# Optimization experiments

Measured on AMD Instinct MI355X. Metric: run time of the kernel, lower is better.

The kernel has to match this reference:

```python
import jax, jax.numpy as jnp
import numpy as np
from jax import lax

NSTEPS = 7
BN_EPS = 1e-5


def setup_inputs() -> dict:
    key = jax.random.key(0)
    ks = jax.random.split(key, 7)
    bs, in_ch, h, w, k = 8, 16, 256, 256, 3
    f = jax.random.normal(ks[0], (bs, in_ch, h, w), dtype=jnp.float32)
    vec_w = jax.random.normal(ks[1], (2 * in_ch, in_ch, k, k), dtype=jnp.float32) * 0.1
    vec_b = jax.random.normal(ks[2], (2 * in_ch,), dtype=jnp.float32) * 0.1
    bn_gamma = jnp.ones((2 * in_ch,), dtype=jnp.float32)
    bn_beta = jnp.zeros((2 * in_ch,), dtype=jnp.float32)
    fuse_w = jax.random.normal(ks[3], (in_ch, in_ch, NSTEPS, 1, 1), dtype=jnp.float32) * 0.1
    fuse_b = jax.random.normal(ks[4], (in_ch,), dtype=jnp.float32) * 0.1
    return {"f": f, "vec_w": vec_w, "vec_b": vec_b, "bn_gamma": bn_gamma,
            "bn_beta": bn_beta, "fuse_w": fuse_w, "fuse_b": fuse_b}


def _bilinear_sample(src, py, px):
    """Bilinear sample with zero padding (torch grid_sample align_corners=True).
    src: [N,C,H,W]; py,px: [N,H,W] pixel coordinates (row, col)."""
    N, C, H, W = src.shape
    y0 = jnp.floor(py); x0 = jnp.floor(px)
    wy1 = py - y0; wy0 = 1.0 - wy1
    wx1 = px - x0; wx0 = 1.0 - wx1
    src_flat = src.reshape(N, C, H * W)

    def gather(yi, xi):
        valid = (yi >= 0) & (yi <= H - 1) & (xi >= 0) & (xi <= W - 1)
        yc = jnp.clip(yi, 0, H - 1).astype(jnp.int32)
        xc = jnp.clip(xi, 0, W - 1).astype(jnp.int32)
        idx = (yc * W + xc).reshape(N, 1, H * W)
        vals = jnp.take_along_axis(src_flat, idx, axis=2).reshape(N, C, H, W)
        return vals * valid.astype(src.dtype)[:, None, :, :]

    out = (wy0 * wx0)[:, None] * gather(y0, x0) \
        + (wy0 * wx1)[:, None] * gather(y0, x0 + 1) \
        + (wy1 * wx0)[:, None] * gather(y0 + 1, x0) \
        + (wy1 * wx1)[:, None] * gather(y0 + 1, x0 + 1)
    return out


def _warp(src, flow, grid_y, grid_x):
    # grid + flow in pixel space; original normalizes to [-1,1] then grid_sample
    # un-normalizes with align_corners=True, which is exactly pixel coords grid+flow.
    py = grid_y[None] + flow[:, 0]
    px = grid_x[None] + flow[:, 1]
    return _bilinear_sample(src, py, px)


def reference(f, vec_w, vec_b, bn_gamma, bn_beta, fuse_w, fuse_b):
    bs, in_ch, h, w = f.shape
    # vec_conv + BatchNorm2d (training-mode batch stats, biased variance)
    vec = lax.conv_general_dilated(f, vec_w, (1, 1), [(1, 1), (1, 1)],
                                   dimension_numbers=("NCHW", "OIHW", "NCHW"))
    vec = vec + vec_b[None, :, None, None]
    mean = vec.mean(axis=(0, 2, 3))
    var = vec.var(axis=(0, 2, 3))
    vec = bn_gamma[None, :, None, None] * (vec - mean[None, :, None, None]) \
        * lax.rsqrt(var + BN_EPS)[None, :, None, None] + bn_beta[None, :, None, None]

    c = vec.shape[1]  # = 2*in_ch
    vec = vec.reshape(bs * c // 2, 2, h, w)  # per-channel 2D flow fields

    grid_y, grid_x = jnp.meshgrid(jnp.arange(h, dtype=f.dtype),
                                  jnp.arange(w, dtype=f.dtype), indexing="ij")

    # VecInt: scaling and squaring, keeping every intermediate deformation
    vec = vec * (1.0 / 2 ** NSTEPS)
    deforms = []
    for _ in range(NSTEPS):
        vec = vec + _warp(vec, vec, grid_y, grid_x)
        deforms.append(vec)

    fsrc = f.reshape(bs * in_ch, 1, h, w)
    maps = [_warp(fsrc, d, grid_y, grid_x).reshape(bs, in_ch, h, w) for d in deforms]
    stacked = jnp.stack(maps, axis=2)  # [bs, in_ch, nsteps, h, w]

    # Conv3d with kernel (nsteps,1,1) then squeeze -> per-pixel channel/step mix
    out = jnp.einsum("ocs,bcshw->bohw", fuse_w[:, :, :, 0, 0], stacked)
    out = out + fuse_b[None, :, None, None]
    return out
```

## Files before the change

kernel.cpp:

```cpp
#include <hip/hip_runtime.h>
#include <hip/hip_fp16.h>

#define H 256
#define W 256
#define BS 8
#define IC 16
#define OCH 32
#define NSTEPS 7
#define PLANE (H*W)
#define NFIELDS (BS*IC)
#define BN_N (BS*PLANE)
#define BN_EPS 1e-5f
#define PW 260
#define PSZ (260 * 260)

__global__ void transpose_w_kernel(const float* __restrict__ w,
                                   __half2* __restrict__ wTh) {
    for (int idx = threadIdx.x; idx < IC * 9 * 16; idx += blockDim.x) {
        int rc = idx >> 4;
        int p  = idx & 15;
        float lo = w[(2 * p) * (IC * 9) + rc];
        float hi = w[(2 * p + 1) * (IC * 9) + rc];
        wTh[idx] = __floats2half2_rn(lo, hi);
    }
}

__global__ void guard_zero_kernel(unsigned* __restrict__ bufA,
                                  unsigned* __restrict__ bufB,
                                  unsigned short* __restrict__ f16p) {
    int p = blockIdx.x;
    size_t pb = (size_t)p * PSZ;
    for (int i = threadIdx.x; i < 2064; i += blockDim.x) {
        int row, col;
        if (i < 1040) {
            int r = i / 260;
            row = (r == 0) ? 0 : 256 + r;
            col = i - r * 260;
        } else {
            int j = i - 1040;
            int c = j / 256;
            col = (c == 0) ? 0 : 256 + c;
            row = 1 + (j - c * 256);
        }
        size_t off = pb + (size_t)row * PW + col;
        bufA[off] = 0u;
        bufB[off] = 0u;
        f16p[off] = 0;
    }
}

__global__ __launch_bounds__(256) void dup_kernel(const float* __restrict__ f,
                                                  __half* __restrict__ f16p) {
    int blk = blockIdx.x;
    int p  = blk >> 3;
    int r0 = (blk & 7) * 32;
    const float* fp = f + (size_t)p * PLANE;
    __half* dp = f16p + (size_t)p * PSZ;
    int tx = threadIdx.x;
#pragma unroll 4
    for (int ry = 0; ry < 32; ++ry) {
        int y = r0 + ry;
        dp[(size_t)(y + 1) * PW + tx + 1] = __float2half(fp[(size_t)y * W + tx]);
    }
}

__global__ __launch_bounds__(256, 8) void conv_kernel(
    const float* __restrict__ f, const __half2* __restrict__ wTh,
    const float* __restrict__ vec_b, __half2* __restrict__ vec_out) {
    __shared__ __align__(16) __half sf[16][10][40];

    int blk = blockIdx.x;
    int xcd = blk & 7;
    int i   = blk >> 3;
    int b   = i >> 5;
    int j   = i & 31;
    int ty0 = ((xcd << 2) | (j >> 3)) * 8;
    int tx0 = (j & 7) * 32;
    int tid = threadIdx.x;

    {
        int sic = tid >> 4;
        int st  = tid & 15;
        if (st < 10) {
            int gx0 = tx0 - 4 + 4 * st;
            const float* fpl = f + (size_t)(b * IC + sic) * PLANE;
            bool full = (gx0 >= 0) && (gx0 + 3 < W);
#pragma unroll
            for (int r = 0; r < 10; ++r) {
                int gy = ty0 - 1 + r;
                float4 v = make_float4(0.f, 0.f, 0.f, 0.f);
                if ((unsigned)gy < (unsigned)H) {
                    if (full) {
                        v = *(const float4*)(fpl + (size_t)gy * W + gx0);
                    } else {
                        if ((unsigned)(gx0 + 0) < (unsigned)W) v.x = fpl[(size_t)gy * W + gx0 + 0];
                        if ((unsigned)(gx0 + 1) < (unsigned)W) v.y = fpl[(size_t)gy * W + gx0 + 1];
                        if ((unsigned)(gx0 + 2) < (unsigned)W) v.z = fpl[(size_t)gy * W + gx0 + 2];
                        if ((unsigned)(gx0 + 3) < (unsigned)W) v.w = fpl[(size_t)gy * W + gx0 + 3];
                    }
                }
                union { __half2 h[2]; float2 f2; } u;
                u.h[0] = __floats2half2_rn(v.x, v.y);
                u.h[1] = __floats2half2_rn(v.z, v.w);
                *(float2*)&sf[sic][r][4 * st] = u.f2;
            }
        }
    }

    __half2 acc[16];
#pragma unroll
    for (int p = 0; p < 16; ++p)
        acc[p] = __floats2half2_rn(vec_b[2 * p], vec_b[2 * p + 1]);

    __syncthreads();

    int tyl = tid >> 5, txl = tid & 31;
#pragma unroll 2
    for (int ic = 0; ic < 16; ++ic) {
#pragma unroll
        for (int k = 0; k < 9; ++k) {
            int ky = k / 3, kx = k - ky * 3;
            __half2 fv = __half2half2(sf[ic][tyl + ky][txl + kx + 3]);
            const __half2* wrow = wTh + (ic * 9 + k) * 16;
#pragma unroll
            for (int p = 0; p < 16; ++p)
                acc[p] = __hfma2(fv, wrow[p], acc[p]);
        }
    }

    int y = ty0 + tyl, x = tx0 + txl;
#pragma unroll
    for (int c = 0; c < IC; ++c)
        vec_out[(size_t)(b * IC + c) * PLANE + (size_t)y * W + x] = acc[c];
}

__global__ __launch_bounds__(256) void stats_kernel(
    const __half2* __restrict__ vec, float* __restrict__ stats) {
    int blk   = blockIdx.x;
    int n     = blk >> 4;
    int chunk = blk & 15;
    const float4* p4 = (const float4*)(vec + (size_t)n * PLANE + chunk * 4096);
    int tid = threadIdx.x;

    float s0 = 0.f, s1 = 0.f, q0 = 0.f, q1 = 0.f;
#pragma unroll 2
    for (int i = tid; i < 1024; i += 256) {
        float4 w = p4[i];
        const __half2* hh = (const __half2*)&w;
#pragma unroll
        for (int q = 0; q < 4; ++q) {
            float2 v = __half22float2(hh[q]);
            s0 += v.x; s1 += v.y;
            q0 = fmaf(v.x, v.x, q0);
            q1 = fmaf(v.y, v.y, q1);
        }
    }
#pragma unroll
    for (int off = 32; off > 0; off >>= 1) {
        s0 += __shfl_down(s0, off, 64);
        s1 += __shfl_down(s1, off, 64);
        q0 += __shfl_down(q0, off, 64);
        q1 += __shfl_down(q1, off, 64);
    }
    __shared__ float red[4][4];
    int wave = tid >> 6, lane = tid & 63;
    if (lane == 0) {
        red[wave][0] = s0; red[wave][1] = s1;
        red[wave][2] = q0; red[wave][3] = q1;
    }
    __syncthreads();
    if (tid == 0) {
        float t0 = 0.f, t1 = 0.f, t2 = 0.f, t3 = 0.f;
#pragma unroll
        for (int wv = 0; wv < 4; ++wv) {
            t0 += red[wv][0]; t1 += red[wv][1];
            t2 += red[wv][2]; t3 += red[wv][3];
        }
        int ch0 = 2 * (n & 15);
        atomicAdd(stats + ch0,          t0);
        atomicAdd(stats + ch0 + 1,      t1);
        atomicAdd(stats + 32 + ch0,     t2);
        atomicAdd(stats + 32 + ch0 + 1, t3);
    }
}

__global__ void finalize_kernel(const float* __restrict__ stats,
                                const float* __restrict__ gamma,
                                const float* __restrict__ beta,
                                float* __restrict__ AB) {
    int ch = threadIdx.x;
    if (ch < 2 * IC) {
        const float invN = 1.f / (float)BN_N;
        float mean = stats[ch] * invN;
        float var  = stats[32 + ch] * invN - mean * mean;
        float rs   = rsqrtf(var + BN_EPS);
        float a    = gamma[ch] * rs;
        AB[ch]      = a * (1.f / 128.f);
        AB[32 + ch] = (beta[ch] - a * mean) * (1.f / 128.f);
    }
}

__device__ __forceinline__ void tap_setup(float py, float px,
                                          int* o, float* wt) {
    float ffy = floorf(py), ffx = floorf(px);
    int y0 = (int)ffy, x0 = (int)ffx;
    float wy1 = py - ffy, wy0 = 1.f - wy1;
    float wx1 = px - ffx, wx0 = 1.f - wx1;
    bool vy0 = (unsigned)y0 < (unsigned)H, vy1 = (unsigned)(y0 + 1) < (unsigned)H;
    bool vx0 = (unsigned)x0 < (unsigned)W, vx1 = (unsigned)(x0 + 1) < (unsigned)W;
    int yc0 = min(max(y0, 0), H - 1), yc1 = min(max(y0 + 1, 0), H - 1);
    int xc0 = min(max(x0, 0), W - 1), xc1 = min(max(x0 + 1, 0), W - 1);
    o[0] = yc0 * W + xc0; o[1] = yc0 * W + xc1;
    o[2] = yc1 * W + xc0; o[3] = yc1 * W + xc1;
    wt[0] = (vy0 && vx0) ? wy0 * wx0 : 0.f;
    wt[1] = (vy0 && vx1) ? wy0 * wx1 : 0.f;
    wt[2] = (vy1 && vx0) ? wy1 * wx0 : 0.f;
    wt[3] = (vy1 && vx1) ? wy1 * wx1 : 0.f;
}

__device__ __forceinline__ void tap_fast(float py, float px,
                                         int& o, float* wt) {
    float pyc = fminf(fmaxf(py, -1.f), 256.f);
    float pxc = fminf(fmaxf(px, -1.f), 256.f);
    float fy = floorf(pyc), fx = floorf(pxc);
    int y0 = (int)fy, x0 = (int)fx;
    float wy1 = pyc - fy, wy0 = 1.f - wy1;
    float wx1 = pxc - fx, wx0 = 1.f - wx1;
    o = (y0 + 1) * PW + (x0 + 1);
    wt[0] = wy0 * wx0; wt[1] = wy0 * wx1;
    wt[2] = wy1 * wx0; wt[3] = wy1 * wx1;
}

template <bool FIRST, bool LAST>
__global__ __launch_bounds__(256, 4) void warp_step(
    const __half2* __restrict__ vinRaw, const __half2* __restrict__ vinPad,
    __half2* __restrict__ voutPad, const __half* __restrict__ f16p,
    const float* __restrict__ AB, __half* __restrict__ mvOut) {
    int blk  = blockIdx.x;
    int fld  = blk & 127;
    int band = blk >> 7;
    int c    = fld & 15;
    int tx   = threadIdx.x;
    const __half2* vinR = FIRST ? vinRaw + (size_t)fld * PLANE : nullptr;
    const __half2* vinP = FIRST ? nullptr : vinPad + (size_t)fld * PSZ;
    __half2* voutP = LAST ? nullptr : voutPad + (size_t)fld * PSZ;
    const __half* fp = f16p + (size_t)fld * PSZ;
    __half* mv = mvOut + (size_t)fld * PLANE;

    float a0 = 0.f, b0 = 0.f, a1 = 0.f, b1 = 0.f;
    if (FIRST) {
        a0 = AB[2 * c];     b0 = AB[32 + 2 * c];
        a1 = AB[2 * c + 1]; b1 = AB[32 + 2 * c + 1];
    }

#pragma unroll 4
    for (int r = 0; r < 8; ++r) {
        int h = band * 8 + r;
        int idx_raw = h * W + tx;
        int idx_pad = (h + 1) * PW + tx + 1;
        float ny, nx;
        if (FIRST) {
            float2 vc = __half22float2(vinR[idx_raw]);
            float fy = fmaf(a0, vc.x, b0);
            float fx = fmaf(a1, vc.y, b1);
            int om[4]; float wt[4];
            tap_setup((float)h + fy, (float)tx + fx, om, wt);
            float2 t0 = __half22float2(vinR[om[0]]);
            float2 t1 = __half22float2(vinR[om[1]]);
            float2 t2 = __half22float2(vinR[om[2]]);
            float2 t3 = __half22float2(vinR[om[3]]);
            float Sy = wt[0] * t0.x + wt[1] * t1.x + wt[2] * t2.x + wt[3] * t3.x;
            float Sx = wt[0] * t0.y + wt[1] * t1.y + wt[2] * t2.y + wt[3] * t3.y;
            float Ws = wt[0] + wt[1] + wt[2] + wt[3];
            ny = fy + fmaf(a0, Sy, b0 * Ws);
            nx = fx + fmaf(a1, Sx, b1 * Ws);
        } else {
            float2 vc = __half22float2(vinP[idx_pad]);
            float fy = vc.x, fx = vc.y;
            int ob; float wt[4];
            tap_fast((float)h + fy, (float)tx + fx, ob, wt);
            union { float2 f2; __half2 hh[2]; } top, bot;
            top.f2 = *reinterpret_cast<const float2*>(vinP + ob);
            bot.f2 = *reinterpret_cast<const float2*>(vinP + ob + PW);
            float2 t0 = __half22float2(top.hh[0]);
            float2 t1 = __half22float2(top.hh[1]);
            float2 t2 = __half22float2(bot.hh[0]);
            float2 t3 = __half22float2(bot.hh[1]);
            ny = fy + wt[0] * t0.x + wt[1] * t1.x + wt[2] * t2.x + wt[3] * t3.x;
            nx = fx + wt[0] * t0.y + wt[1] * t1.y + wt[2] * t2.y + wt[3] * t3.y;
        }
        if (!LAST)
            voutP[idx_pad] = __float22half2_rn(make_float2(ny, nx));
        int pb; float pw[4];
        tap_fast((float)h + ny, (float)tx + nx, pb, pw);
        union { float f; __half2 h2; } r0u, r1u;
        r0u.f = *reinterpret_cast<const float*>(fp + pb);
        r1u.f = *reinterpret_cast<const float*>(fp + pb + PW);
        float2 g0 = __half22float2(r0u.h2);
        float2 g1 = __half22float2(r1u.h2);
        float m = pw[0] * g0.x + pw[1] * g0.y + pw[2] * g1.x + pw[3] * g1.y;
        mv[idx_raw] = __float2half(m);
    }
}

__global__ __launch_bounds__(256) void mix_kernel(
    const __half* __restrict__ mvs,
    const __half* __restrict__ mv6,
    const float* __restrict__ fw, const float* __restrict__ fb,
    float* __restrict__ out) {
    int blk = blockIdx.x;
    int b   = blk >> 8;
    int h   = blk & 255;
    int tx  = threadIdx.x;
    int idx = h * W + tx;

    float acc[IC];
#pragma unroll
    for (int o = 0; o < IC; ++o) acc[o] = fb[o];

#pragma unroll
    for (int s = 0; s < NSTEPS; ++s) {
        const __half* base = (s < NSTEPS - 1)
            ? mvs + (size_t)s * NFIELDS * PLANE : mv6;
#pragma unroll
        for (int c = 0; c < IC; ++c) {
            float m = __half2float(base[(size_t)(b * IC + c) * PLANE + idx]);
#pragma unroll
            for (int o = 0; o < IC; ++o)
                acc[o] = fmaf(fw[(o * IC + c) * NSTEPS + s], m, acc[o]);
        }
    }

#pragma unroll
    for (int o = 0; o < IC; ++o)
        out[(size_t)(b * IC + o) * PLANE + idx] = acc[o];
}

template <bool FIRST, bool LAST>
__global__ __launch_bounds__(256) void step_kernel(
    const __half2* __restrict__ vinRaw, const __half2* __restrict__ vinPad,
    __half2* __restrict__ voutPad, const __half* __restrict__ f16p,
    const float* __restrict__ AB, const float* __restrict__ fw,
    const float* __restrict__ fb, __half* __restrict__ accp,
    float* __restrict__ out, int step) {
    int blk = blockIdx.x;
    int xcd = blk & 7;
    int i   = blk >> 3;
    int b   = i >> 5;
    int h   = (xcd << 5) | (i & 31);
    int tx  = threadIdx.x;
    int idx_raw = h * W + tx;
    int idx_pad = (h + 1) * PW + tx + 1;
    const size_t baseR = (size_t)b * IC * PLANE;
    const size_t baseP = (size_t)b * IC * PSZ;

    float mv[IC];

#pragma unroll 2
    for (int g = 0; g < 4; ++g) {
        float a0j[4], b0j[4], a1j[4], b1j[4];
        float fy[4], fx[4];
        float wt[4][4];
        int   ob[4];
        int   om[4][4];
        const __half2* pl[4];
        float2 vc[4];

#pragma unroll
        for (int j = 0; j < 4; ++j) {
            int c = 4 * g + j;
            if (FIRST) {
                pl[j] = vinRaw + baseR + (size_t)c * PLANE;
                vc[j] = __half22float2(pl[j][idx_raw]);
            } else {
                pl[j] = vinPad + baseP + (size_t)c * PSZ;
                vc[j] = __half22float2(pl[j][idx_pad]);
            }
        }

#pragma unroll
        for (int j = 0; j < 4; ++j) {
            int c = 4 * g + j;
            if (FIRST) {
                a0j[j] = AB[2 * c];     b0j[j] = AB[32 + 2 * c];
                a1j[j] = AB[2 * c + 1]; b1j[j] = AB[32 + 2 * c + 1];
                fy[j] = fmaf(a0j[j], vc[j].x, b0j[j]);
                fx[j] = fmaf(a1j[j], vc[j].y, b1j[j]);
                tap_setup((float)h + fy[j], (float)tx + fx[j], om[j], wt[j]);
            } else {
                fy[j] = vc[j].x;
                fx[j] = vc[j].y;
                tap_fast((float)h + fy[j], (float)tx + fx[j], ob[j], wt[j]);
            }
        }

        float2 t[4][4];
#pragma unroll
        for (int j = 0; j < 4; ++j) {
            if (FIRST) {
#pragma unroll
                for (int k = 0; k < 4; ++k)
                    t[j][k] = __half22float2(pl[j][om[j][k]]);
            } else {
                union { float2 f2; __half2 hh[2]; } top, bot;
                top.f2 = *reinterpret_cast<const float2*>(pl[j] + ob[j]);
                bot.f2 = *reinterpret_cast<const float2*>(pl[j] + ob[j] + PW);
                t[j][0] = __half22float2(top.hh[0]);
                t[j][1] = __half22float2(top.hh[1]);
                t[j][2] = __half22float2(bot.hh[0]);
                t[j][3] = __half22float2(bot.hh[1]);
            }
        }

        float ny[4], nx[4];
        int   pb_[4];
        float pw_[4][4];
#pragma unroll
        for (int j = 0; j < 4; ++j) {
            int c = 4 * g + j;
            float Sy = wt[j][0] * t[j][0].x + wt[j][1] * t[j][1].x
                     + wt[j][2] * t[j][2].x + wt[j][3] * t[j][3].x;
            float Sx = wt[j][0] * t[j][0].y + wt[j][1] * t[j][1].y
                     + wt[j][2] * t[j][2].y + wt[j][3] * t[j][3].y;
            if (FIRST) {
                float Ws = wt[j][0] + wt[j][1] + wt[j][2] + wt[j][3];
                ny[j] = fy[j] + fmaf(a0j[j], Sy, b0j[j] * Ws);
                nx[j] = fx[j] + fmaf(a1j[j], Sx, b1j[j] * Ws);
            } else {
                ny[j] = fy[j] + Sy;
                nx[j] = fx[j] + Sx;
            }
            if (!LAST)
                voutPad[baseP + (size_t)c * PSZ + idx_pad] =
                    __float22half2_rn(make_float2(ny[j], nx[j]));
            tap_fast((float)h + ny[j], (float)tx + nx[j], pb_[j], pw_[j]);
        }

#pragma unroll
        for (int j = 0; j < 4; ++j) {
            int c = 4 * g + j;
            const __half* fp = f16p + baseP + (size_t)c * PSZ;
            union { float f; __half2 h; } r0, r1;
            r0.f = *reinterpret_cast<const float*>(fp + pb_[j]);
            r1.f = *reinterpret_cast<const float*>(fp + pb_[j] + PW);
            float2 g0 = __half22float2(r0.h);
            float2 g1 = __half22float2(r1.h);
            mv[c] = pw_[j][0] * g0.x + pw_[j][1] * g0.y
                  + pw_[j][2] * g1.x + pw_[j][3] * g1.y;
        }
    }

    __half* ap = accp + ((size_t)b * PLANE + idx_raw) * IC;
    float prev[IC];
    if (!FIRST) {
        float4 p0 = ((const float4*)ap)[0];
        float4 p1 = ((const float4*)ap)[1];
        const __half2* ph = (const __half2*)&p0;
#pragma unroll
        for (int k = 0; k < 4; ++k) {
            float2 v = __half22float2(ph[k]);
            prev[2 * k] = v.x; prev[2 * k + 1] = v.y;
        }
        const __half2* qh = (const __half2*)&p1;
#pragma unroll
        for (int k = 0; k < 4; ++k) {
            float2 v = __half22float2(qh[k]);
            prev[8 + 2 * k] = v.x; prev[8 + 2 * k + 1] = v.y;
        }
    }

    float a[IC];
#pragma unroll
    for (int o2 = 0; o2 < IC; ++o2) {
        a[o2] = FIRST ? fb[o2] : prev[o2];
#pragma unroll
        for (int c = 0; c < IC; ++c)
            a[o2] = fmaf(fw[(o2 * IC + c) * NSTEPS + step], mv[c], a[o2]);
    }

    if (LAST) {
#pragma unroll
        for (int o2 = 0; o2 < IC; ++o2)
            out[baseR + (size_t)o2 * PLANE + idx_raw] = a[o2];
    } else {
        float4 s0, s1;
        __half2* sh = (__half2*)&s0;
#pragma unroll
        for (int k = 0; k < 4; ++k)
            sh[k] = __float22half2_rn(make_float2(a[2 * k], a[2 * k + 1]));
        __half2* th = (__half2*)&s1;
#pragma unroll
        for (int k = 0; k < 4; ++k)
            th[k] = __float22half2_rn(make_float2(a[8 + 2 * k], a[9 + 2 * k]));
        ((float4*)ap)[0] = s0;
        ((float4*)ap)[1] = s1;
    }
}

extern "C" void kernel_launch(void* const* d_in, const int* in_sizes, int n_in,
                              void* d_out, int out_size, void* d_ws,
                              size_t ws_size, hipStream_t stream) {
    const float* f      = (const float*)d_in[0];
    const float* vec_w  = (const float*)d_in[1];
    const float* vec_b  = (const float*)d_in[2];
    const float* gamma  = (const float*)d_in[3];
    const float* beta   = (const float*)d_in[4];
    const float* fuse_w = (const float*)d_in[5];
    const float* fuse_b = (const float*)d_in[6];
    float* out = (float*)d_out;

    char* ws = (char*)d_ws;
    const size_t rawB   = (size_t)NFIELDS * PLANE * sizeof(__half2);
    const size_t padB2  = (size_t)NFIELDS * PSZ * sizeof(__half2);
    const size_t padB1  = (size_t)NFIELDS * PSZ * sizeof(__half);
    const size_t planeH = (size_t)NFIELDS * PLANE * sizeof(__half);
    const size_t smallB = 16384;
    __half2* bufRaw = (__half2*)ws;
    __half2* bufA   = (__half2*)(ws + rawB);
    __half2* bufB   = (__half2*)(ws + rawB + padB2);
    __half*  f16p   = (__half*)(ws + rawB + 2 * padB2);
    char*    smallp = ws + rawB + 2 * padB2 + padB1;
    __half2* wTh    = (__half2*)smallp;
    float*   stats  = (float*)(smallp + 10240);
    float*   AB     = (float*)(smallp + 10240 + 256);
    char*    regionX = smallp + smallB;
    __half*  mvs    = (__half*)regionX;
    __half*  accp   = (__half*)regionX;

    const size_t need_new = rawB + 2 * padB2 + padB1 + smallB
                          + (size_t)(NSTEPS - 1) * planeH;
    const bool use_new = (ws_size >= need_new);

    hipMemsetAsync(stats, 0, 64 * sizeof(float), stream);
    transpose_w_kernel<<<1, 512, 0, stream>>>(vec_w, wTh);
    guard_zero_kernel<<<NFIELDS, 256, 0, stream>>>(
        (unsigned*)bufA, (unsigned*)bufB, (unsigned short*)f16p);
    dup_kernel<<<NFIELDS * 8, 256, 0, stream>>>(f, f16p);
    conv_kernel<<<2048, 256, 0, stream>>>(f, wTh, vec_b, bufRaw);
    stats_kernel<<<NFIELDS * 16, 256, 0, stream>>>(bufRaw, stats);
    finalize_kernel<<<1, 64, 0, stream>>>(stats, gamma, beta, AB);

    if (use_new) {
        for (int s = 0; s < NSTEPS; ++s) {
            const __half2* vinPad = (s & 1) ? bufA : bufB;
            __half2*       voutP  = (s & 1) ? bufB : bufA;
            __half* mvP = (s < NSTEPS - 1) ? mvs + (size_t)s * NFIELDS * PLANE
                                           : (__half*)bufRaw;
            if (s == 0)
                warp_step<true, false><<<4096, 256, 0, stream>>>(
                    bufRaw, (const __half2*)nullptr, bufA, f16p, AB, mvP);
            else if (s < NSTEPS - 1)
                warp_step<false, false><<<4096, 256, 0, stream>>>(
                    (const __half2*)nullptr, vinPad, voutP, f16p, AB, mvP);
            else
                warp_step<false, true><<<4096, 256, 0, stream>>>(
                    (const __half2*)nullptr, vinPad, (__half2*)nullptr, f16p,
                    AB, mvP);
        }
        mix_kernel<<<2048, 256, 0, stream>>>(
            mvs, (const __half*)bufRaw, fuse_w, fuse_b, out);
    } else {
        for (int s = 0; s < NSTEPS; ++s) {
            const __half2* vinPad = (s & 1) ? bufA : bufB;
            __half2*       voutP  = (s & 1) ? bufB : bufA;
            if (s == 0)
                step_kernel<true, false><<<2048, 256, 0, stream>>>(
                    bufRaw, (const __half2*)nullptr, bufA, f16p, AB,
                    fuse_w, fuse_b, accp, out, s);
            else if (s < NSTEPS - 1)
                step_kernel<false, false><<<2048, 256, 0, stream>>>(
                    (const __half2*)nullptr, vinPad, voutP, f16p, AB,
                    fuse_w, fuse_b, accp, out, s);
            else
                step_kernel<false, true><<<2048, 256, 0, stream>>>(
                    (const __half2*)nullptr, vinPad, (__half2*)nullptr, f16p,
                    AB, fuse_w, fuse_b, accp, out, s);
        }
    }
}
```

Before: 580.5 us.

## Process fields in two halves to keep intermediates L2/MALL-resident and vectorize mix

Splits the 128 flow fields into two halves of 64, running the seven warp steps and the mix kernel per half. Each per-step map buffer is therefore half the size, which keeps the working set smaller and more cache-resident and shrinks the required workspace. The step_kernel fallback and the workspace-size check are removed. The mix kernel now handles two pixels per thread with half2 loads and float2 stores. In exchange there are twice as many launches, each with half the grid, which may lower occupancy per launch.

```diff
diff --git a/kernel.cpp b/kernel.cpp
--- a/kernel.cpp
+++ b/kernel.cpp
@@ -235,17 +235,18 @@
 __global__ __launch_bounds__(256, 4) void warp_step(
     const __half2* __restrict__ vinRaw, const __half2* __restrict__ vinPad,
     __half2* __restrict__ voutPad, const __half* __restrict__ f16p,
-    const float* __restrict__ AB, __half* __restrict__ mvOut) {
+    const float* __restrict__ AB, __half* __restrict__ mvOut, int f0) {
     int blk  = blockIdx.x;
-    int fld  = blk & 127;
-    int band = blk >> 7;
+    int fldl = blk & 63;
+    int band = blk >> 6;
+    int fld  = f0 + fldl;
     int c    = fld & 15;
     int tx   = threadIdx.x;
     const __half2* vinR = FIRST ? vinRaw + (size_t)fld * PLANE : nullptr;
     const __half2* vinP = FIRST ? nullptr : vinPad + (size_t)fld * PSZ;
     __half2* voutP = LAST ? nullptr : voutPad + (size_t)fld * PSZ;
     const __half* fp = f16p + (size_t)fld * PSZ;
-    __half* mv = mvOut + (size_t)fld * PLANE;
+    __half* mv = mvOut + (size_t)fldl * PLANE;
 
     float a0 = 0.f, b0 = 0.f, a1 = 0.f, b1 = 0.f;
     if (FIRST) {
@@ -307,194 +308,45 @@
     const __half* __restrict__ mvs,
     const __half* __restrict__ mv6,
     const float* __restrict__ fw, const float* __restrict__ fb,
-    float* __restrict__ out) {
+    float* __restrict__ out, int b0) {
     int blk = blockIdx.x;
-    int b   = blk >> 8;
-    int h   = blk & 255;
-    int tx  = threadIdx.x;
-    int idx = h * W + tx;
-
-    float acc[IC];
-#pragma unroll
-    for (int o = 0; o < IC; ++o) acc[o] = fb[o];
+    int bl  = blk >> 7;
+    int hp  = blk & 127;
+    int tid = threadIdx.x;
+    int h   = hp * 2 + (tid >> 7);
+    int px  = (tid & 127) << 1;
+    int idx = h * W + px;
+
+    float ax[IC], ay[IC];
+#pragma unroll
+    for (int o = 0; o < IC; ++o) { ax[o] = fb[o]; ay[o] = fb[o]; }
 
 #pragma unroll
     for (int s = 0; s < NSTEPS; ++s) {
         const __half* base = (s < NSTEPS - 1)
-            ? mvs + (size_t)s * NFIELDS * PLANE : mv6;
+            ? mvs + ((size_t)s * 64 + (size_t)bl * IC) * PLANE
+            : mv6 + (size_t)bl * IC * PLANE;
+        __half2 m2[IC];
+#pragma unroll
+        for (int c = 0; c < IC; ++c)
+            m2[c] = *reinterpret_cast<const __half2*>(base + (size_t)c * PLANE + idx);
 #pragma unroll
         for (int c = 0; c < IC; ++c) {
-            float m = __half2float(base[(size_t)(b * IC + c) * PLANE + idx]);
-#pragma unroll
-            for (int o = 0; o < IC; ++o)
-                acc[o] = fmaf(fw[(o * IC + c) * NSTEPS + s], m, acc[o]);
-        }
-    }
-
+            float2 m = __half22float2(m2[c]);
+#pragma unroll
+            for (int o = 0; o < IC; ++o) {
+                float w = fw[(o * IC + c) * NSTEPS + s];
+                ax[o] = fmaf(w, m.x, ax[o]);
+                ay[o] = fmaf(w, m.y, ay[o]);
+            }
+        }
+    }
+
+    int b = b0 + bl;
 #pragma unroll
     for (int o = 0; o < IC; ++o)
-        out[(size_t)(b * IC + o) * PLANE + idx] = acc[o];
-}
-
-template <bool FIRST, bool LAST>
-__global__ __launch_bounds__(256) void step_kernel(
-    const __half2* __restrict__ vinRaw, const __half2* __restrict__ vinPad,
-    __half2* __restrict__ voutPad, const __half* __restrict__ f16p,
-    const float* __restrict__ AB, const float* __restrict__ fw,
-    const float* __restrict__ fb, __half* __restrict__ accp,
-    float* __restrict__ out, int step) {
-    int blk = blockIdx.x;
-    int xcd = blk & 7;
-    int i   = blk >> 3;
-    int b   = i >> 5;
-    int h   = (xcd << 5) | (i & 31);
-    int tx  = threadIdx.x;
-    int idx_raw = h * W + tx;
-    int idx_pad = (h + 1) * PW + tx + 1;
-    const size_t baseR = (size_t)b * IC * PLANE;
-    const size_t baseP = (size_t)b * IC * PSZ;
-
-    float mv[IC];
-
-#pragma unroll 2
-    for (int g = 0; g < 4; ++g) {
-        float a0j[4], b0j[4], a1j[4], b1j[4];
-        float fy[4], fx[4];
-        float wt[4][4];
-        int   ob[4];
-        int   om[4][4];
-        const __half2* pl[4];
-        float2 vc[4];
-
-#pragma unroll
-        for (int j = 0; j < 4; ++j) {
-            int c = 4 * g + j;
-            if (FIRST) {
-                pl[j] = vinRaw + baseR + (size_t)c * PLANE;
-                vc[j] = __half22float2(pl[j][idx_raw]);
-            } else {
-                pl[j] = vinPad + baseP + (size_t)c * PSZ;
-                vc[j] = __half22float2(pl[j][idx_pad]);
-            }
-        }
-
-#pragma unroll
-        for (int j = 0; j < 4; ++j) {
-            int c = 4 * g + j;
-            if (FIRST) {
-                a0j[j] = AB[2 * c];     b0j[j] = AB[32 + 2 * c];
-                a1j[j] = AB[2 * c + 1]; b1j[j] = AB[32 + 2 * c + 1];
-                fy[j] = fmaf(a0j[j], vc[j].x, b0j[j]);
-                fx[j] = fmaf(a1j[j], vc[j].y, b1j[j]);
-                tap_setup((float)h + fy[j], (float)tx + fx[j], om[j], wt[j]);
-            } else {
-                fy[j] = vc[j].x;
-                fx[j] = vc[j].y;
-                tap_fast((float)h + fy[j], (float)tx + fx[j], ob[j], wt[j]);
-            }
-        }
-
-        float2 t[4][4];
-#pragma unroll
-        for (int j = 0; j < 4; ++j) {
-            if (FIRST) {
-#pragma unroll
-                for (int k = 0; k < 4; ++k)
-                    t[j][k] = __half22float2(pl[j][om[j][k]]);
-            } else {
-                union { float2 f2; __half2 hh[2]; } top, bot;
-                top.f2 = *reinterpret_cast<const float2*>(pl[j] + ob[j]);
-                bot.f2 = *reinterpret_cast<const float2*>(pl[j] + ob[j] + PW);
-                t[j][0] = __half22float2(top.hh[0]);
-                t[j][1] = __half22float2(top.hh[1]);
-                t[j][2] = __half22float2(bot.hh[0]);
-                t[j][3] = __half22float2(bot.hh[1]);
-            }
-        }
-
-        float ny[4], nx[4];
-        int   pb_[4];
-        float pw_[4][4];
-#pragma unroll
-        for (int j = 0; j < 4; ++j) {
-            int c = 4 * g + j;
-            float Sy = wt[j][0] * t[j][0].x + wt[j][1] * t[j][1].x
-                     + wt[j][2] * t[j][2].x + wt[j][3] * t[j][3].x;
-            float Sx = wt[j][0] * t[j][0].y + wt[j][1] * t[j][1].y
-                     + wt[j][2] * t[j][2].y + wt[j][3] * t[j][3].y;
-            if (FIRST) {
-                float Ws = wt[j][0] + wt[j][1] + wt[j][2] + wt[j][3];
-                ny[j] = fy[j] + fmaf(a0j[j], Sy, b0j[j] * Ws);
-                nx[j] = fx[j] + fmaf(a1j[j], Sx, b1j[j] * Ws);
-            } else {
-                ny[j] = fy[j] + Sy;
-                nx[j] = fx[j] + Sx;
-            }
-            if (!LAST)
-                voutPad[baseP + (size_t)c * PSZ + idx_pad] =
-                    __float22half2_rn(make_float2(ny[j], nx[j]));
-            tap_fast((float)h + ny[j], (float)tx + nx[j], pb_[j], pw_[j]);
-        }
-
-#pragma unroll
-        for (int j = 0; j < 4; ++j) {
-            int c = 4 * g + j;
-            const __half* fp = f16p + baseP + (size_t)c * PSZ;
-            union { float f; __half2 h; } r0, r1;
-            r0.f = *reinterpret_cast<const float*>(fp + pb_[j]);
-            r1.f = *reinterpret_cast<const float*>(fp + pb_[j] + PW);
-            float2 g0 = __half22float2(r0.h);
-            float2 g1 = __half22float2(r1.h);
-            mv[c] = pw_[j][0] * g0.x + pw_[j][1] * g0.y
-                  + pw_[j][2] * g1.x + pw_[j][3] * g1.y;
-        }
-    }
-
-    __half* ap = accp + ((size_t)b * PLANE + idx_raw) * IC;
-    float prev[IC];
-    if (!FIRST) {
-        float4 p0 = ((const float4*)ap)[0];
-        float4 p1 = ((const float4*)ap)[1];
-        const __half2* ph = (const __half2*)&p0;
-#pragma unroll
-        for (int k = 0; k < 4; ++k) {
-            float2 v = __half22float2(ph[k]);
-            prev[2 * k] = v.x; prev[2 * k + 1] = v.y;
-        }
-        const __half2* qh = (const __half2*)&p1;
-#pragma unroll
-        for (int k = 0; k < 4; ++k) {
-            float2 v = __half22float2(qh[k]);
-            prev[8 + 2 * k] = v.x; prev[8 + 2 * k + 1] = v.y;
-        }
-    }
-
-    float a[IC];
-#pragma unroll
-    for (int o2 = 0; o2 < IC; ++o2) {
-        a[o2] = FIRST ? fb[o2] : prev[o2];
-#pragma unroll
-        for (int c = 0; c < IC; ++c)
-            a[o2] = fmaf(fw[(o2 * IC + c) * NSTEPS + step], mv[c], a[o2]);
-    }
-
-    if (LAST) {
-#pragma unroll
-        for (int o2 = 0; o2 < IC; ++o2)
-            out[baseR + (size_t)o2 * PLANE + idx_raw] = a[o2];
-    } else {
-        float4 s0, s1;
-        __half2* sh = (__half2*)&s0;
-#pragma unroll
-        for (int k = 0; k < 4; ++k)
-            sh[k] = __float22half2_rn(make_float2(a[2 * k], a[2 * k + 1]));
-        __half2* th = (__half2*)&s1;
-#pragma unroll
-        for (int k = 0; k < 4; ++k)
-            th[k] = __float22half2_rn(make_float2(a[8 + 2 * k], a[9 + 2 * k]));
-        ((float4*)ap)[0] = s0;
-        ((float4*)ap)[1] = s1;
-    }
+        *reinterpret_cast<float2*>(out + (size_t)(b * IC + o) * PLANE + idx)
+            = make_float2(ax[o], ay[o]);
 }
 
 extern "C" void kernel_launch(void* const* d_in, const int* in_sizes, int n_in,
@@ -513,7 +365,6 @@
     const size_t rawB   = (size_t)NFIELDS * PLANE * sizeof(__half2);
     const size_t padB2  = (size_t)NFIELDS * PSZ * sizeof(__half2);
     const size_t padB1  = (size_t)NFIELDS * PSZ * sizeof(__half);
-    const size_t planeH = (size_t)NFIELDS * PLANE * sizeof(__half);
     const size_t smallB = 16384;
     __half2* bufRaw = (__half2*)ws;
     __half2* bufA   = (__half2*)(ws + rawB);
@@ -523,13 +374,7 @@
     __half2* wTh    = (__half2*)smallp;
     float*   stats  = (float*)(smallp + 10240);
     float*   AB     = (float*)(smallp + 10240 + 256);
-    char*    regionX = smallp + smallB;
-    __half*  mvs    = (__half*)regionX;
-    __half*  accp   = (__half*)regionX;
-
-    const size_t need_new = rawB + 2 * padB2 + padB1 + smallB
-                          + (size_t)(NSTEPS - 1) * planeH;
-    const bool use_new = (ws_size >= need_new);
+    __half*  mvs    = (__half*)(smallp + smallB);
 
     hipMemsetAsync(stats, 0, 64 * sizeof(float), stream);
     transpose_w_kernel<<<1, 512, 0, stream>>>(vec_w, wTh);
@@ -540,41 +385,28 @@
     stats_kernel<<<NFIELDS * 16, 256, 0, stream>>>(bufRaw, stats);
     finalize_kernel<<<1, 64, 0, stream>>>(stats, gamma, beta, AB);
 
-    if (use_new) {
+    const size_t mvHalf = (size_t)64 * PLANE;
+    for (int hf = 0; hf < 2; ++hf) {
+        int f0 = hf * 64;
         for (int s = 0; s < NSTEPS; ++s) {
             const __half2* vinPad = (s & 1) ? bufA : bufB;
             __half2*       voutP  = (s & 1) ? bufB : bufA;
-            __half* mvP = (s < NSTEPS - 1) ? mvs + (size_t)s * NFIELDS * PLANE
-                                           : (__half*)bufRaw;
+            __half* mvP = (s < NSTEPS - 1)
+                ? mvs + (size_t)s * mvHalf
+                : (__half*)bufRaw + (size_t)f0 * PLANE;
             if (s == 0)
-                warp_step<true, false><<<4096, 256, 0, stream>>>(
-                    bufRaw, (const __half2*)nullptr, bufA, f16p, AB, mvP);
+                warp_step<true, false><<<2048, 256, 0, stream>>>(
+                    bufRaw, (const __half2*)nullptr, bufA, f16p, AB, mvP, f0);
             else if (s < NSTEPS - 1)
-                warp_step<false, false><<<4096, 256, 0, stream>>>(
-                    (const __half2*)nullptr, vinPad, voutP, f16p, AB, mvP);
+                warp_step<false, false><<<2048, 256, 0, stream>>>(
+                    (const __half2*)nullptr, vinPad, voutP, f16p, AB, mvP, f0);
             else
-                warp_step<false, true><<<4096, 256, 0, stream>>>(
+                warp_step<false, true><<<2048, 256, 0, stream>>>(
                     (const __half2*)nullptr, vinPad, (__half2*)nullptr, f16p,
-                    AB, mvP);
-        }
-        mix_kernel<<<2048, 256, 0, stream>>>(
-            mvs, (const __half*)bufRaw, fuse_w, fuse_b, out);
-    } else {
-        for (int s = 0; s < NSTEPS; ++s) {
-            const __half2* vinPad = (s & 1) ? bufA : bufB;
-            __half2*       voutP  = (s & 1) ? bufB : bufA;
-            if (s == 0)
-                step_kernel<true, false><<<2048, 256, 0, stream>>>(
-                    bufRaw, (const __half2*)nullptr, bufA, f16p, AB,
-                    fuse_w, fuse_b, accp, out, s);
-            else if (s < NSTEPS - 1)
-                step_kernel<false, false><<<2048, 256, 0, stream>>>(
-                    (const __half2*)nullptr, vinPad, voutP, f16p, AB,
-                    fuse_w, fuse_b, accp, out, s);
-            else
-                step_kernel<false, true><<<2048, 256, 0, stream>>>(
-                    (const __half2*)nullptr, vinPad, (__half2*)nullptr, f16p,
-                    AB, fuse_w, fuse_b, accp, out, s);
-        }
-    }
-}
+                    AB, mvP, f0);
+        }
+        mix_kernel<<<512, 256, 0, stream>>>(
+            mvs, (const __half*)bufRaw + (size_t)f0 * PLANE,
+            fuse_w, fuse_b, out, f0 >> 4);
+    }
+}
```

New measurement: 694.3 us. +19.6%, slower.
